# Kernel tuning notes

Measured on AMD Instinct MI355X. Metric: run time of the kernel, lower is better.

## Reference

```python
import jax, jax.numpy as jnp
import numpy as np

N_NODES = 100000
N_EDGES = 1600000
D = 64


def setup_inputs() -> dict:
    key = jax.random.key(0)
    k1, k2, k3 = jax.random.split(key, 3)
    z = jax.random.normal(k1, (N_NODES, D), dtype=jnp.float32)
    ei = jax.random.randint(k2, (2, N_EDGES), 0, N_NODES, dtype=jnp.int32)
    W = jax.random.normal(k3, (D, D), dtype=jnp.float32) * (1.0 / np.sqrt(D))
    b = jnp.zeros((D,), dtype=jnp.float32)
    return {"z": z, "ei": ei, "W": W, "b": b}


def reference(z, ei, W, b):
    # PyG GCNConv(64,64) with default add_self_loops=True, normalize=True, bias,
    # followed by ReLU (from StructDec.forward).
    N = z.shape[0]
    loops = jnp.arange(N, dtype=ei.dtype)
    src = jnp.concatenate([ei[0], loops])  # [E+N]
    dst = jnp.concatenate([ei[1], loops])  # [E+N]

    # symmetric normalization: deg computed on dst with unit edge weights
    deg = jax.ops.segment_sum(jnp.ones_like(dst, dtype=z.dtype), dst, num_segments=N)
    dinv = jnp.where(deg > 0, jax.lax.rsqrt(deg), 0.0)  # deg >= 1 due to self-loops
    norm = dinv[src] * dinv[dst]  # [E+N]

    # linear transform first (small GEMM), then gather-scale-scatter
    x = z @ W.T  # [N, D]
    msg = x[src] * norm[:, None]  # [E+N, D]
    out = jax.ops.segment_sum(msg, dst, num_segments=N) + b  # [N, D]
    return jax.nn.relu(out)
```

## Files before the change

### kernel.cpp

```cpp
#include <hip/hip_runtime.h>

#define DD 64
#define BSH 7
#define GBKT 128
#define CAP 2560
#define TILE 8192
#define PTHREADS 1024
#define EPT 8
#define MAXBK 1024

__device__ __forceinline__ float bflo(unsigned int u) {
    return __uint_as_float(u << 16);
}
__device__ __forceinline__ float bfhi(unsigned int u) {
    return __uint_as_float(u & 0xffff0000u);
}
__device__ __forceinline__ unsigned short f2bf(float f) {
    unsigned int b = __float_as_uint(f);
    return (unsigned short)((b + 0x7fffu + ((b >> 16) & 1u)) >> 16);
}
__device__ __forceinline__ void acc_row(uint4 r, float4& lo, float4& hi) {
    lo.x += bflo(r.x); lo.y += bfhi(r.x);
    lo.z += bflo(r.y); lo.w += bfhi(r.y);
    hi.x += bflo(r.z); hi.y += bfhi(r.z);
    hi.z += bflo(r.w); hi.w += bfhi(r.w);
}

__global__ __launch_bounds__(PTHREADS) void part_k(const int* __restrict__ src,
                                                   const int* __restrict__ dst,
                                                   int* __restrict__ bcur,
                                                   int* __restrict__ bp,
                                                   int E, int NBK) {
    __shared__ int hist[MAXBK];
    __shared__ int scanb[MAXBK];
    __shared__ int gbase[MAXBK];
    __shared__ int stage[TILE];
    __shared__ unsigned short bstage[TILE];

    int tid = threadIdx.x;
    int tbase = blockIdx.x * TILE;
    int n = E - tbase;
    if (n > TILE) n = TILE;

    for (int i = tid; i < NBK; i += PTHREADS) hist[i] = 0;
    __syncthreads();

    int ss[EPT], dd[EPT];
    int eb = tid * EPT;
    bool dal = ((reinterpret_cast<size_t>(dst) & 15) == 0);
    if (dal && eb + EPT <= n) {
        const int4* s4 = (const int4*)(src + tbase + eb);
        const int4* d4 = (const int4*)(dst + tbase + eb);
        int4 a = s4[0], b2 = s4[1], c4 = d4[0], e4 = d4[1];
        ss[0] = a.x; ss[1] = a.y; ss[2] = a.z; ss[3] = a.w;
        ss[4] = b2.x; ss[5] = b2.y; ss[6] = b2.z; ss[7] = b2.w;
        dd[0] = c4.x; dd[1] = c4.y; dd[2] = c4.z; dd[3] = c4.w;
        dd[4] = e4.x; dd[5] = e4.y; dd[6] = e4.z; dd[7] = e4.w;
    } else {
        #pragma unroll
        for (int e = 0; e < EPT; ++e) {
            if (eb + e < n) { ss[e] = src[tbase + eb + e]; dd[e] = dst[tbase + eb + e]; }
            else dd[e] = -1;
        }
    }
    int pv[EPT], pb[EPT], pr[EPT];
    #pragma unroll
    for (int e = 0; e < EPT; ++e) {
        pb[e] = -1;
        if (eb + e < n && dd[e] >= 0) {
            pv[e] = (ss[e] << BSH) | (dd[e] & (GBKT - 1));
            pb[e] = dd[e] >> BSH;
            pr[e] = atomicAdd(&hist[pb[e]], 1);
        }
    }
    __syncthreads();

    if (tid < 64) {
        int run = 0;
        for (int base = 0; base < NBK; base += 64) {
            int i = base + tid;
            int orig = (i < NBK) ? hist[i] : 0;
            int v = orig;
            #pragma unroll
            for (int off = 1; off < 64; off <<= 1) {
                int t = __shfl_up(v, off, 64);
                if (tid >= off) v += t;
            }
            if (i < NBK) scanb[i] = run + v - orig;
            run += __shfl(v, 63, 64);
        }
    }
    __syncthreads();

    for (int i = tid; i < NBK; i += PTHREADS)
        if (hist[i]) gbase[i] = i * CAP + atomicAdd(&bcur[i], hist[i]);
    #pragma unroll
    for (int e = 0; e < EPT; ++e) {
        if (pb[e] >= 0) {
            int p = scanb[pb[e]] + pr[e];
            stage[p] = pv[e];
            bstage[p] = (unsigned short)pb[e];
        }
    }
    __syncthreads();

    for (int i = tid; i < n; i += PTHREADS) {
        int b = bstage[i];
        bp[gbase[b] + (i - scanb[b])] = stage[i];
    }
}

__global__ __launch_bounds__(512) void dg_k(const int* __restrict__ bp,
                                            const int* __restrict__ bcur,
                                            const float* __restrict__ z,
                                            const float* __restrict__ W,
                                            ushort4* __restrict__ ybf, int N) {
    __shared__ float Wt[64 * 68];
    __shared__ float zt[32 * 68];
    __shared__ int cnt[GBKT];
    __shared__ float dinvL[GBKT];
    int k = blockIdx.x;
    int tid = threadIdx.x;
    int base = k << BSH;

    if (tid < GBKT) cnt[tid] = 0;
    for (int i = tid; i < DD * DD; i += 512) {
        int d = i >> 6, kk = i & 63;
        Wt[kk * 68 + d] = W[i];
    }
    __syncthreads();
    {
        int ebeg = k * CAP;
        int eend = ebeg + bcur[k];
        for (int i = ebeg + tid; i < eend; i += 512)
            atomicAdd(&cnt[bp[i] & (GBKT - 1)], 1);
    }
    __syncthreads();
    if (tid < GBKT) dinvL[tid] = rsqrtf((float)(1 + cnt[tid]));
    for (int it = 0; it < 4; ++it) {
        __syncthreads();
        int rl = it * 32 + (tid >> 4);
        int row = base + rl;
        float4 v = (row < N) ? ((const float4*)z)[(size_t)row * 16 + (tid & 15)]
                             : make_float4(0.f, 0.f, 0.f, 0.f);
        *(float4*)&zt[(tid >> 4) * 68 + (tid & 15) * 4] = v;
        __syncthreads();
        int r = tid >> 4, c = tid & 15;
        float4 acc = make_float4(0.f, 0.f, 0.f, 0.f);
        #pragma unroll
        for (int kk = 0; kk < DD; ++kk) {
            float zv = zt[r * 68 + kk];
            float4 w = *(const float4*)&Wt[kk * 68 + c * 4];
            acc.x = fmaf(zv, w.x, acc.x);
            acc.y = fmaf(zv, w.y, acc.y);
            acc.z = fmaf(zv, w.z, acc.z);
            acc.w = fmaf(zv, w.w, acc.w);
        }
        if (row < N) {
            float s = dinvL[rl];
            ushort4 o;
            o.x = f2bf(acc.x * s);
            o.y = f2bf(acc.y * s);
            o.z = f2bf(acc.z * s);
            o.w = f2bf(acc.w * s);
            ybf[(size_t)row * 16 + c] = o;
        }
    }
}

__global__ __launch_bounds__(256) void bg_k(const uint4* __restrict__ ybf,
                                            const int* __restrict__ bp,
                                            const int* __restrict__ bcur,
                                            const float4* __restrict__ b4,
                                            float4* __restrict__ out4, int N) {
    __shared__ int cnt[GBKT];
    __shared__ int excl[GBKT];
    __shared__ int cur[GBKT];
    __shared__ int sorted[CAP];
    __shared__ int nextn;
    int k = blockIdx.x;
    int tid = threadIdx.x;
    int ebeg = k * CAP;
    int eend = ebeg + bcur[k];
    int base = k << BSH;

    if (tid < GBKT) cnt[tid] = 0;
    if (tid == 0) nextn = 0;
    __syncthreads();
    int ev[10];
    #pragma unroll
    for (int u = 0; u < 10; ++u) {
        int i = ebeg + tid + u * 256;
        ev[u] = (i < eend) ? bp[i] : -1;
    }
    #pragma unroll
    for (int u = 0; u < 10; ++u)
        if (ev[u] >= 0) atomicAdd(&cnt[ev[u] & (GBKT - 1)], 1);
    __syncthreads();

    if (tid < GBKT) excl[tid] = cnt[tid];
    __syncthreads();
    #pragma unroll
    for (int off = 1; off < GBKT; off <<= 1) {
        int t = (tid < GBKT && tid >= off) ? excl[tid - off] : 0;
        __syncthreads();
        if (tid < GBKT) excl[tid] += t;
        __syncthreads();
    }
    if (tid < GBKT) {
        excl[tid] -= cnt[tid];
        cur[tid] = excl[tid];
    }
    __syncthreads();

    #pragma unroll
    for (int u = 0; u < 10; ++u)
        if (ev[u] >= 0) {
            int l = ev[u] & (GBKT - 1);
            int pos = atomicAdd(&cur[l], 1);
            sorted[pos] = ev[u] >> BSH;
        }
    __syncthreads();

    int lane = tid & 63;
    int c = tid & 7;
    for (;;) {
        int slot;
        if ((tid & 7) == 0) slot = atomicAdd(&nextn, 1);
        slot = __shfl(slot, lane & 56, 64);
        if (slot >= GBKT) break;
        int node = base + slot;
        if (node >= N) continue;
        int beg = excl[slot];
        int cn = cnt[slot];
        int end = beg + cn;
        uint4 v = ybf[(size_t)node * 8 + c];
        float4 a0 = make_float4(bflo(v.x), bfhi(v.x), bflo(v.y), bfhi(v.y));
        float4 a1 = make_float4(bflo(v.z), bfhi(v.z), bflo(v.w), bfhi(v.w));
        float4 e0 = make_float4(0.f, 0.f, 0.f, 0.f);
        float4 e1 = e0;
        int j = beg;
        for (; j + 7 < end; j += 8) {
            int s0 = sorted[j],     s1 = sorted[j + 1], s2 = sorted[j + 2], s3 = sorted[j + 3];
            int s4 = sorted[j + 4], s5 = sorted[j + 5], s6 = sorted[j + 6], s7 = sorted[j + 7];
            uint4 r0 = ybf[(size_t)s0 * 8 + c];
            uint4 r1 = ybf[(size_t)s1 * 8 + c];
            uint4 r2 = ybf[(size_t)s2 * 8 + c];
            uint4 r3 = ybf[(size_t)s3 * 8 + c];
            uint4 r4 = ybf[(size_t)s4 * 8 + c];
            uint4 r5 = ybf[(size_t)s5 * 8 + c];
            uint4 r6 = ybf[(size_t)s6 * 8 + c];
            uint4 r7 = ybf[(size_t)s7 * 8 + c];
            acc_row(r0, a0, a1);
            acc_row(r1, e0, e1);
            acc_row(r2, a0, a1);
            acc_row(r3, e0, e1);
            acc_row(r4, a0, a1);
            acc_row(r5, e0, e1);
            acc_row(r6, a0, a1);
            acc_row(r7, e0, e1);
        }
        for (; j + 3 < end; j += 4) {
            int s0 = sorted[j], s1 = sorted[j + 1], s2 = sorted[j + 2], s3 = sorted[j + 3];
            uint4 r0 = ybf[(size_t)s0 * 8 + c];
            uint4 r1 = ybf[(size_t)s1 * 8 + c];
            uint4 r2 = ybf[(size_t)s2 * 8 + c];
            uint4 r3 = ybf[(size_t)s3 * 8 + c];
            acc_row(r0, a0, a1);
            acc_row(r1, e0, e1);
            acc_row(r2, a0, a1);
            acc_row(r3, e0, e1);
        }
        for (; j < end; ++j) {
            uint4 r = ybf[(size_t)sorted[j] * 8 + c];
            acc_row(r, a0, a1);
        }
        a0.x += e0.x; a0.y += e0.y; a0.z += e0.z; a0.w += e0.w;
        a1.x += e1.x; a1.y += e1.y; a1.z += e1.z; a1.w += e1.w;

        float dn = rsqrtf((float)(1 + cn));
        float4 bb0 = b4[2 * c];
        float4 bb1 = b4[2 * c + 1];
        float4 o0, o1;
        o0.x = fmaxf(fmaf(a0.x, dn, bb0.x), 0.f);
        o0.y = fmaxf(fmaf(a0.y, dn, bb0.y), 0.f);
        o0.z = fmaxf(fmaf(a0.z, dn, bb0.z), 0.f);
        o0.w = fmaxf(fmaf(a0.w, dn, bb0.w), 0.f);
        o1.x = fmaxf(fmaf(a1.x, dn, bb1.x), 0.f);
        o1.y = fmaxf(fmaf(a1.y, dn, bb1.y), 0.f);
        o1.z = fmaxf(fmaf(a1.z, dn, bb1.z), 0.f);
        o1.w = fmaxf(fmaf(a1.w, dn, bb1.w), 0.f);
        out4[(size_t)node * 16 + 2 * c] = o0;
        out4[(size_t)node * 16 + 2 * c + 1] = o1;
    }
}


extern "C" void kernel_launch(void* const* d_in, const int* in_sizes, int n_in,
                              void* d_out, int out_size, void* d_ws, size_t ws_size,
                              hipStream_t stream) {
    const float* z = (const float*)d_in[0];
    const int* ei  = (const int*)d_in[1];
    const float* W = (const float*)d_in[2];
    const float* b = (const float*)d_in[3];
    float* out = (float*)d_out;

    const int N = in_sizes[0] / DD;
    const int E = in_sizes[1] / 2;
    const int* src = ei;
    const int* dst = ei + E;

    const int NBK = (N + GBKT - 1) >> BSH;

    unsigned short* ybf = (unsigned short*)d_ws;
    int*   bcur  = (int*)(ybf + (size_t)64 * N);
    int*   bp    = bcur + NBK;

    hipMemsetAsync(bcur, 0, sizeof(int) * NBK, stream);
    part_k<<<(E + TILE - 1) / TILE, PTHREADS, 0, stream>>>(src, dst, bcur, bp, E, NBK);
    dg_k<<<NBK, 512, 0, stream>>>(bp, bcur, z, W, (ushort4*)ybf, N);
    bg_k<<<NBK, 256, 0, stream>>>((const uint4*)ybf, bp, bcur,
                                  (const float4*)b, (float4*)out, N);
}
```

Before: 87.33 us.

## Fuse partition, transform and gather into one cooperative persistent kernel

Merges the memset, partition, degree+GEMM and gather stages into a single cooperative kernel that uses grid-wide syncs between phases. Shared memory is reused through a union, and persistent blocks loop over tiles and buckets. The partition tile is halved with more edges per thread. The aim is to remove launch gaps and tail effects between the four launches. In exchange, grid.sync costs are added and occupancy is limited to co-resident blocks. The original multi-kernel path remains as a fallback when the cooperative launch fails.

```diff
diff --git a/kernel.cpp b/kernel.cpp
--- a/kernel.cpp
+++ b/kernel.cpp
@@ -1,13 +1,19 @@
 #include <hip/hip_runtime.h>
+#include <hip/hip_cooperative_groups.h>
+
+namespace cg = cooperative_groups;
 
 #define DD 64
 #define BSH 7
 #define GBKT 128
 #define CAP 2560
-#define TILE 8192
-#define PTHREADS 1024
-#define EPT 8
-#define MAXBK 1024
+#define MAXBK 800
+
+#define FTILE 8192
+#define FPT 1024
+#define FEPT 8
+#define MTILE 4096
+#define MEPT 16
 
 __device__ __forceinline__ float bflo(unsigned int u) {
     return __uint_as_float(u << 16);
@@ -26,166 +32,22 @@
     hi.z += bflo(r.w); hi.w += bfhi(r.w);
 }
 
-__global__ __launch_bounds__(PTHREADS) void part_k(const int* __restrict__ src,
-                                                   const int* __restrict__ dst,
-                                                   int* __restrict__ bcur,
-                                                   int* __restrict__ bp,
-                                                   int E, int NBK) {
-    __shared__ int hist[MAXBK];
-    __shared__ int scanb[MAXBK];
-    __shared__ int gbase[MAXBK];
-    __shared__ int stage[TILE];
-    __shared__ unsigned short bstage[TILE];
-
-    int tid = threadIdx.x;
-    int tbase = blockIdx.x * TILE;
-    int n = E - tbase;
-    if (n > TILE) n = TILE;
-
-    for (int i = tid; i < NBK; i += PTHREADS) hist[i] = 0;
-    __syncthreads();
-
-    int ss[EPT], dd[EPT];
-    int eb = tid * EPT;
-    bool dal = ((reinterpret_cast<size_t>(dst) & 15) == 0);
-    if (dal && eb + EPT <= n) {
-        const int4* s4 = (const int4*)(src + tbase + eb);
-        const int4* d4 = (const int4*)(dst + tbase + eb);
-        int4 a = s4[0], b2 = s4[1], c4 = d4[0], e4 = d4[1];
-        ss[0] = a.x; ss[1] = a.y; ss[2] = a.z; ss[3] = a.w;
-        ss[4] = b2.x; ss[5] = b2.y; ss[6] = b2.z; ss[7] = b2.w;
-        dd[0] = c4.x; dd[1] = c4.y; dd[2] = c4.z; dd[3] = c4.w;
-        dd[4] = e4.x; dd[5] = e4.y; dd[6] = e4.z; dd[7] = e4.w;
-    } else {
-        #pragma unroll
-        for (int e = 0; e < EPT; ++e) {
-            if (eb + e < n) { ss[e] = src[tbase + eb + e]; dd[e] = dst[tbase + eb + e]; }
-            else dd[e] = -1;
-        }
-    }
-    int pv[EPT], pb[EPT], pr[EPT];
-    #pragma unroll
-    for (int e = 0; e < EPT; ++e) {
-        pb[e] = -1;
-        if (eb + e < n && dd[e] >= 0) {
-            pv[e] = (ss[e] << BSH) | (dd[e] & (GBKT - 1));
-            pb[e] = dd[e] >> BSH;
-            pr[e] = atomicAdd(&hist[pb[e]], 1);
-        }
-    }
-    __syncthreads();
-
-    if (tid < 64) {
-        int run = 0;
-        for (int base = 0; base < NBK; base += 64) {
-            int i = base + tid;
-            int orig = (i < NBK) ? hist[i] : 0;
-            int v = orig;
-            #pragma unroll
-            for (int off = 1; off < 64; off <<= 1) {
-                int t = __shfl_up(v, off, 64);
-                if (tid >= off) v += t;
-            }
-            if (i < NBK) scanb[i] = run + v - orig;
-            run += __shfl(v, 63, 64);
-        }
-    }
-    __syncthreads();
-
-    for (int i = tid; i < NBK; i += PTHREADS)
-        if (hist[i]) gbase[i] = i * CAP + atomicAdd(&bcur[i], hist[i]);
-    #pragma unroll
-    for (int e = 0; e < EPT; ++e) {
-        if (pb[e] >= 0) {
-            int p = scanb[pb[e]] + pr[e];
-            stage[p] = pv[e];
-            bstage[p] = (unsigned short)pb[e];
-        }
-    }
-    __syncthreads();
-
-    for (int i = tid; i < n; i += PTHREADS) {
-        int b = bstage[i];
-        bp[gbase[b] + (i - scanb[b])] = stage[i];
-    }
-}
-
-__global__ __launch_bounds__(512) void dg_k(const int* __restrict__ bp,
-                                            const int* __restrict__ bcur,
-                                            const float* __restrict__ z,
-                                            const float* __restrict__ W,
-                                            ushort4* __restrict__ ybf, int N) {
-    __shared__ float Wt[64 * 68];
-    __shared__ float zt[32 * 68];
-    __shared__ int cnt[GBKT];
-    __shared__ float dinvL[GBKT];
-    int k = blockIdx.x;
-    int tid = threadIdx.x;
-    int base = k << BSH;
-
-    if (tid < GBKT) cnt[tid] = 0;
-    for (int i = tid; i < DD * DD; i += 512) {
-        int d = i >> 6, kk = i & 63;
-        Wt[kk * 68 + d] = W[i];
-    }
-    __syncthreads();
-    {
-        int ebeg = k * CAP;
-        int eend = ebeg + bcur[k];
-        for (int i = ebeg + tid; i < eend; i += 512)
-            atomicAdd(&cnt[bp[i] & (GBKT - 1)], 1);
-    }
-    __syncthreads();
-    if (tid < GBKT) dinvL[tid] = rsqrtf((float)(1 + cnt[tid]));
-    for (int it = 0; it < 4; ++it) {
-        __syncthreads();
-        int rl = it * 32 + (tid >> 4);
-        int row = base + rl;
-        float4 v = (row < N) ? ((const float4*)z)[(size_t)row * 16 + (tid & 15)]
-                             : make_float4(0.f, 0.f, 0.f, 0.f);
-        *(float4*)&zt[(tid >> 4) * 68 + (tid & 15) * 4] = v;
-        __syncthreads();
-        int r = tid >> 4, c = tid & 15;
-        float4 acc = make_float4(0.f, 0.f, 0.f, 0.f);
-        #pragma unroll
-        for (int kk = 0; kk < DD; ++kk) {
-            float zv = zt[r * 68 + kk];
-            float4 w = *(const float4*)&Wt[kk * 68 + c * 4];
-            acc.x = fmaf(zv, w.x, acc.x);
-            acc.y = fmaf(zv, w.y, acc.y);
-            acc.z = fmaf(zv, w.z, acc.z);
-            acc.w = fmaf(zv, w.w, acc.w);
-        }
-        if (row < N) {
-            float s = dinvL[rl];
-            ushort4 o;
-            o.x = f2bf(acc.x * s);
-            o.y = f2bf(acc.y * s);
-            o.z = f2bf(acc.z * s);
-            o.w = f2bf(acc.w * s);
-            ybf[(size_t)row * 16 + c] = o;
-        }
-    }
-}
-
-__global__ __launch_bounds__(256) void bg_k(const uint4* __restrict__ ybf,
-                                            const int* __restrict__ bp,
-                                            const int* __restrict__ bcur,
-                                            const float4* __restrict__ b4,
-                                            float4* __restrict__ out4, int N) {
-    __shared__ int cnt[GBKT];
-    __shared__ int excl[GBKT];
-    __shared__ int cur[GBKT];
-    __shared__ int sorted[CAP];
-    __shared__ int nextn;
-    int k = blockIdx.x;
+struct SMb {
+    int cnt[GBKT]; int excl[GBKT]; int cur[GBKT];
+    int sorted[CAP]; int nextn;
+};
+
+__device__ __forceinline__ void bg_body(SMb& s, const uint4* __restrict__ ybf,
+                                        const int* __restrict__ bp, int count,
+                                        const float4* __restrict__ b4,
+                                        float4* __restrict__ out4, int N, int k) {
     int tid = threadIdx.x;
     int ebeg = k * CAP;
-    int eend = ebeg + bcur[k];
+    int eend = ebeg + count;
     int base = k << BSH;
 
-    if (tid < GBKT) cnt[tid] = 0;
-    if (tid == 0) nextn = 0;
+    if (tid < GBKT) s.cnt[tid] = 0;
+    if (tid == 0) s.nextn = 0;
     __syncthreads();
     int ev[10];
     #pragma unroll
@@ -195,30 +57,28 @@
     }
     #pragma unroll
     for (int u = 0; u < 10; ++u)
-        if (ev[u] >= 0) atomicAdd(&cnt[ev[u] & (GBKT - 1)], 1);
-    __syncthreads();
-
-    if (tid < GBKT) excl[tid] = cnt[tid];
+        if (ev[u] >= 0) atomicAdd(&s.cnt[ev[u] & (GBKT - 1)], 1);
+    __syncthreads();
+    if (tid < GBKT) s.excl[tid] = s.cnt[tid];
     __syncthreads();
     #pragma unroll
     for (int off = 1; off < GBKT; off <<= 1) {
-        int t = (tid < GBKT && tid >= off) ? excl[tid - off] : 0;
-        __syncthreads();
-        if (tid < GBKT) excl[tid] += t;
+        int t = (tid < GBKT && tid >= off) ? s.excl[tid - off] : 0;
+        __syncthreads();
+        if (tid < GBKT) s.excl[tid] += t;
         __syncthreads();
     }
     if (tid < GBKT) {
-        excl[tid] -= cnt[tid];
-        cur[tid] = excl[tid];
-    }
-    __syncthreads();
-
+        s.excl[tid] -= s.cnt[tid];
+        s.cur[tid] = s.excl[tid];
+    }
+    __syncthreads();
     #pragma unroll
     for (int u = 0; u < 10; ++u)
         if (ev[u] >= 0) {
             int l = ev[u] & (GBKT - 1);
-            int pos = atomicAdd(&cur[l], 1);
-            sorted[pos] = ev[u] >> BSH;
+            int pos = atomicAdd(&s.cur[l], 1);
+            s.sorted[pos] = ev[u] >> BSH;
         }
     __syncthreads();
 
@@ -226,13 +86,13 @@
     int c = tid & 7;
     for (;;) {
         int slot;
-        if ((tid & 7) == 0) slot = atomicAdd(&nextn, 1);
+        if ((tid & 7) == 0) slot = atomicAdd(&s.nextn, 1);
         slot = __shfl(slot, lane & 56, 64);
         if (slot >= GBKT) break;
         int node = base + slot;
         if (node >= N) continue;
-        int beg = excl[slot];
-        int cn = cnt[slot];
+        int beg = s.excl[slot];
+        int cn = s.cnt[slot];
         int end = beg + cn;
         uint4 v = ybf[(size_t)node * 8 + c];
         float4 a0 = make_float4(bflo(v.x), bfhi(v.x), bflo(v.y), bfhi(v.y));
@@ -241,8 +101,8 @@
         float4 e1 = e0;
         int j = beg;
         for (; j + 7 < end; j += 8) {
-            int s0 = sorted[j],     s1 = sorted[j + 1], s2 = sorted[j + 2], s3 = sorted[j + 3];
-            int s4 = sorted[j + 4], s5 = sorted[j + 5], s6 = sorted[j + 6], s7 = sorted[j + 7];
+            int s0 = s.sorted[j],     s1 = s.sorted[j + 1], s2 = s.sorted[j + 2], s3 = s.sorted[j + 3];
+            int s4 = s.sorted[j + 4], s5 = s.sorted[j + 5], s6 = s.sorted[j + 6], s7 = s.sorted[j + 7];
             uint4 r0 = ybf[(size_t)s0 * 8 + c];
             uint4 r1 = ybf[(size_t)s1 * 8 + c];
             uint4 r2 = ybf[(size_t)s2 * 8 + c];
@@ -261,7 +121,7 @@
             acc_row(r7, e0, e1);
         }
         for (; j + 3 < end; j += 4) {
-            int s0 = sorted[j], s1 = sorted[j + 1], s2 = sorted[j + 2], s3 = sorted[j + 3];
+            int s0 = s.sorted[j], s1 = s.sorted[j + 1], s2 = s.sorted[j + 2], s3 = s.sorted[j + 3];
             uint4 r0 = ybf[(size_t)s0 * 8 + c];
             uint4 r1 = ybf[(size_t)s1 * 8 + c];
             uint4 r2 = ybf[(size_t)s2 * 8 + c];
@@ -272,7 +132,7 @@
             acc_row(r3, e0, e1);
         }
         for (; j < end; ++j) {
-            uint4 r = ybf[(size_t)sorted[j] * 8 + c];
+            uint4 r = ybf[(size_t)s.sorted[j] * 8 + c];
             acc_row(r, a0, a1);
         }
         a0.x += e0.x; a0.y += e0.y; a0.z += e0.z; a0.w += e0.w;
@@ -295,30 +155,360 @@
     }
 }
 
+struct SMp {
+    int hist[MAXBK]; int scanb[MAXBK]; int gbase[MAXBK];
+    int stage[MTILE]; unsigned short bstage[MTILE];
+};
+struct SMg {
+    float Wt[64 * 68]; float zt[16 * 68];
+    int cnt[GBKT]; float dinvL[GBKT];
+};
+union SMu { SMp p; SMg g; SMb b; };
+
+__global__ __launch_bounds__(256, 4) void mega2_k(
+    const int* __restrict__ src, const int* __restrict__ dst,
+    const float* __restrict__ z, const float* __restrict__ W,
+    const float4* __restrict__ b4, ushort4* __restrict__ ybf,
+    int* __restrict__ bcur, int* __restrict__ bp,
+    float4* __restrict__ out4, int N, int E, int NBK, int nt)
+{
+    __shared__ SMu sm;
+    cg::grid_group grid = cg::this_grid();
+    int tid = threadIdx.x;
+    int bid = blockIdx.x;
+    int G = gridDim.x;
+
+    for (int i = bid * 256 + tid; i < NBK; i += G * 256) bcur[i] = 0;
+    grid.sync();
+
+    for (int t = bid; t < nt; t += G) {
+        int tbase = t * MTILE;
+        int n = E - tbase;
+        if (n > MTILE) n = MTILE;
+        __syncthreads();
+        for (int i = tid; i < NBK; i += 256) sm.p.hist[i] = 0;
+        __syncthreads();
+        int pv[MEPT], pb[MEPT], pr[MEPT];
+        int eb = tid * MEPT;
+        bool full = (eb + MEPT <= n);
+        if (full) {
+            #pragma unroll
+            for (int q = 0; q < MEPT / 4; ++q) {
+                int4 s4 = *(const int4*)(src + tbase + eb + q * 4);
+                int4 d4 = *(const int4*)(dst + tbase + eb + q * 4);
+                int sa[4] = {s4.x, s4.y, s4.z, s4.w};
+                int da[4] = {d4.x, d4.y, d4.z, d4.w};
+                #pragma unroll
+                for (int u = 0; u < 4; ++u) {
+                    int e = q * 4 + u;
+                    pv[e] = (sa[u] << BSH) | (da[u] & (GBKT - 1));
+                    pb[e] = da[u] >> BSH;
+                    pr[e] = atomicAdd(&sm.p.hist[pb[e]], 1);
+                }
+            }
+        } else {
+            #pragma unroll
+            for (int e = 0; e < MEPT; ++e) {
+                pb[e] = -1;
+                if (eb + e < n) {
+                    int s = src[tbase + eb + e];
+                    int d = dst[tbase + eb + e];
+                    pv[e] = (s << BSH) | (d & (GBKT - 1));
+                    pb[e] = d >> BSH;
+                    pr[e] = atomicAdd(&sm.p.hist[pb[e]], 1);
+                }
+            }
+        }
+        __syncthreads();
+        if (tid < 64) {
+            int run = 0;
+            for (int base = 0; base < NBK; base += 64) {
+                int i = base + tid;
+                int orig = (i < NBK) ? sm.p.hist[i] : 0;
+                int v = orig;
+                #pragma unroll
+                for (int off = 1; off < 64; off <<= 1) {
+                    int t2 = __shfl_up(v, off, 64);
+                    if (tid >= off) v += t2;
+                }
+                if (i < NBK) sm.p.scanb[i] = run + v - orig;
+                run += __shfl(v, 63, 64);
+            }
+        }
+        __syncthreads();
+        for (int i = tid; i < NBK; i += 256)
+            if (sm.p.hist[i]) sm.p.gbase[i] = i * CAP + atomicAdd(&bcur[i], sm.p.hist[i]);
+        #pragma unroll
+        for (int e = 0; e < MEPT; ++e) {
+            if (pb[e] >= 0) {
+                int p = sm.p.scanb[pb[e]] + pr[e];
+                sm.p.stage[p] = pv[e];
+                sm.p.bstage[p] = (unsigned short)pb[e];
+            }
+        }
+        __syncthreads();
+        for (int i = tid; i < n; i += 256) {
+            int b = sm.p.bstage[i];
+            bp[sm.p.gbase[b] + (i - sm.p.scanb[b])] = sm.p.stage[i];
+        }
+    }
+    grid.sync();
+
+    for (int i = tid; i < DD * DD; i += 256) {
+        int d = i >> 6, kk = i & 63;
+        sm.g.Wt[kk * 68 + d] = W[i];
+    }
+    for (int k = bid; k < NBK; k += G) {
+        __syncthreads();
+        if (tid < GBKT) sm.g.cnt[tid] = 0;
+        __syncthreads();
+        {
+            int ebeg = k * CAP;
+            int eend = ebeg + bcur[k];
+            for (int i = ebeg + tid; i < eend; i += 256)
+                atomicAdd(&sm.g.cnt[bp[i] & (GBKT - 1)], 1);
+        }
+        __syncthreads();
+        if (tid < GBKT) sm.g.dinvL[tid] = rsqrtf((float)(1 + sm.g.cnt[tid]));
+        int base = k << BSH;
+        for (int it = 0; it < 8; ++it) {
+            __syncthreads();
+            int rl = it * 16 + (tid >> 4);
+            int row = base + rl;
+            float4 v = (row < N) ? ((const float4*)z)[(size_t)row * 16 + (tid & 15)]
+                                 : make_float4(0.f, 0.f, 0.f, 0.f);
+            *(float4*)&sm.g.zt[(tid >> 4) * 68 + (tid & 15) * 4] = v;
+            __syncthreads();
+            int r = tid >> 4, c = tid & 15;
+            float4 acc = make_float4(0.f, 0.f, 0.f, 0.f);
+            #pragma unroll
+            for (int kk = 0; kk < DD; ++kk) {
+                float zv = sm.g.zt[r * 68 + kk];
+                float4 w = *(const float4*)&sm.g.Wt[kk * 68 + c * 4];
+                acc.x = fmaf(zv, w.x, acc.x);
+                acc.y = fmaf(zv, w.y, acc.y);
+                acc.z = fmaf(zv, w.z, acc.z);
+                acc.w = fmaf(zv, w.w, acc.w);
+            }
+            if (row < N) {
+                float s = sm.g.dinvL[rl];
+                ushort4 o;
+                o.x = f2bf(acc.x * s);
+                o.y = f2bf(acc.y * s);
+                o.z = f2bf(acc.z * s);
+                o.w = f2bf(acc.w * s);
+                ybf[(size_t)row * 16 + c] = o;
+            }
+        }
+    }
+    grid.sync();
+
+    for (int k = bid; k < NBK; k += G) {
+        __syncthreads();
+        bg_body(sm.b, (const uint4*)ybf, bp, bcur[k], b4, out4, N, k);
+    }
+}
+
+__global__ __launch_bounds__(FPT) void part_k(const int* __restrict__ src,
+                                              const int* __restrict__ dst,
+                                              int* __restrict__ bcur,
+                                              int* __restrict__ bp,
+                                              int E, int NBK) {
+    __shared__ int hist[MAXBK];
+    __shared__ int scanb[MAXBK];
+    __shared__ int gbase[MAXBK];
+    __shared__ int stage[FTILE];
+    __shared__ unsigned short bstage[FTILE];
+
+    int tid = threadIdx.x;
+    int tbase = blockIdx.x * FTILE;
+    int n = E - tbase;
+    if (n > FTILE) n = FTILE;
+
+    for (int i = tid; i < NBK; i += FPT) hist[i] = 0;
+    __syncthreads();
+
+    int ss[FEPT], dd[FEPT];
+    int eb = tid * FEPT;
+    if (eb + FEPT <= n) {
+        const int4* s4 = (const int4*)(src + tbase + eb);
+        const int4* d4 = (const int4*)(dst + tbase + eb);
+        int4 a = s4[0], b2 = s4[1], c4 = d4[0], e4 = d4[1];
+        ss[0] = a.x; ss[1] = a.y; ss[2] = a.z; ss[3] = a.w;
+        ss[4] = b2.x; ss[5] = b2.y; ss[6] = b2.z; ss[7] = b2.w;
+        dd[0] = c4.x; dd[1] = c4.y; dd[2] = c4.z; dd[3] = c4.w;
+        dd[4] = e4.x; dd[5] = e4.y; dd[6] = e4.z; dd[7] = e4.w;
+    } else {
+        #pragma unroll
+        for (int e = 0; e < FEPT; ++e) {
+            if (eb + e < n) { ss[e] = src[tbase + eb + e]; dd[e] = dst[tbase + eb + e]; }
+            else dd[e] = -1;
+        }
+    }
+    int pv[FEPT], pb[FEPT], pr[FEPT];
+    #pragma unroll
+    for (int e = 0; e < FEPT; ++e) {
+        pb[e] = -1;
+        if (eb + e < n && dd[e] >= 0) {
+            pv[e] = (ss[e] << BSH) | (dd[e] & (GBKT - 1));
+            pb[e] = dd[e] >> BSH;
+            pr[e] = atomicAdd(&hist[pb[e]], 1);
+        }
+    }
+    __syncthreads();
+
+    if (tid < 64) {
+        int run = 0;
+        for (int base = 0; base < NBK; base += 64) {
+            int i = base + tid;
+            int orig = (i < NBK) ? hist[i] : 0;
+            int v = orig;
+            #pragma unroll
+            for (int off = 1; off < 64; off <<= 1) {
+                int t = __shfl_up(v, off, 64);
+                if (tid >= off) v += t;
+            }
+            if (i < NBK) scanb[i] = run + v - orig;
+            run += __shfl(v, 63, 64);
+        }
+    }
+    __syncthreads();
+
+    for (int i = tid; i < NBK; i += FPT)
+        if (hist[i]) gbase[i] = i * CAP + atomicAdd(&bcur[i], hist[i]);
+    #pragma unroll
+    for (int e = 0; e < FEPT; ++e) {
+        if (pb[e] >= 0) {
+            int p = scanb[pb[e]] + pr[e];
+            stage[p] = pv[e];
+            bstage[p] = (unsigned short)pb[e];
+        }
+    }
+    __syncthreads();
+
+    for (int i = tid; i < n; i += FPT) {
+        int b = bstage[i];
+        bp[gbase[b] + (i - scanb[b])] = stage[i];
+    }
+}
+
+__global__ __launch_bounds__(512) void dg_k(const int* __restrict__ bp,
+                                            const int* __restrict__ bcur,
+                                            const float* __restrict__ z,
+                                            const float* __restrict__ W,
+                                            ushort4* __restrict__ ybf, int N) {
+    __shared__ float Wt[64 * 68];
+    __shared__ float zt[32 * 68];
+    __shared__ int cnt[GBKT];
+    __shared__ float dinvL[GBKT];
+    int k = blockIdx.x;
+    int tid = threadIdx.x;
+    int base = k << BSH;
+
+    if (tid < GBKT) cnt[tid] = 0;
+    for (int i = tid; i < DD * DD; i += 512) {
+        int d = i >> 6, kk = i & 63;
+        Wt[kk * 68 + d] = W[i];
+    }
+    __syncthreads();
+    {
+        int ebeg = k * CAP;
+        int eend = ebeg + bcur[k];
+        for (int i = ebeg + tid; i < eend; i += 512)
+            atomicAdd(&cnt[bp[i] & (GBKT - 1)], 1);
+    }
+    __syncthreads();
+    if (tid < GBKT) dinvL[tid] = rsqrtf((float)(1 + cnt[tid]));
+    for (int it = 0; it < 4; ++it) {
+        __syncthreads();
+        int rl = it * 32 + (tid >> 4);
+        int row = base + rl;
+        float4 v = (row < N) ? ((const float4*)z)[(size_t)row * 16 + (tid & 15)]
+                             : make_float4(0.f, 0.f, 0.f, 0.f);
+        *(float4*)&zt[(tid >> 4) * 68 + (tid & 15) * 4] = v;
+        __syncthreads();
+        int r = tid >> 4, c = tid & 15;
+        float4 acc = make_float4(0.f, 0.f, 0.f, 0.f);
+        #pragma unroll
+        for (int kk = 0; kk < DD; ++kk) {
+            float zv = zt[r * 68 + kk];
+            float4 w = *(const float4*)&Wt[kk * 68 + c * 4];
+            acc.x = fmaf(zv, w.x, acc.x);
+            acc.y = fmaf(zv, w.y, acc.y);
+            acc.z = fmaf(zv, w.z, acc.z);
+            acc.w = fmaf(zv, w.w, acc.w);
+        }
+        if (row < N) {
+            float s = dinvL[rl];
+            ushort4 o;
+            o.x = f2bf(acc.x * s);
+            o.y = f2bf(acc.y * s);
+            o.z = f2bf(acc.z * s);
+            o.w = f2bf(acc.w * s);
+            ybf[(size_t)row * 16 + c] = o;
+        }
+    }
+}
+
+__global__ __launch_bounds__(256) void bg_k(const uint4* __restrict__ ybf,
+                                            const int* __restrict__ bp,
+                                            const int* __restrict__ bcur,
+                                            const float4* __restrict__ b4,
+                                            float4* __restrict__ out4, int N) {
+    __shared__ SMb s;
+    bg_body(s, ybf, bp, bcur[blockIdx.x], b4, out4, N, blockIdx.x);
+}
 
 extern "C" void kernel_launch(void* const* d_in, const int* in_sizes, int n_in,
                               void* d_out, int out_size, void* d_ws, size_t ws_size,
                               hipStream_t stream) {
-    const float* z = (const float*)d_in[0];
-    const int* ei  = (const int*)d_in[1];
-    const float* W = (const float*)d_in[2];
-    const float* b = (const float*)d_in[3];
-    float* out = (float*)d_out;
-
-    const int N = in_sizes[0] / DD;
-    const int E = in_sizes[1] / 2;
-    const int* src = ei;
-    const int* dst = ei + E;
-
-    const int NBK = (N + GBKT - 1) >> BSH;
-
-    unsigned short* ybf = (unsigned short*)d_ws;
-    int*   bcur  = (int*)(ybf + (size_t)64 * N);
-    int*   bp    = bcur + NBK;
-
-    hipMemsetAsync(bcur, 0, sizeof(int) * NBK, stream);
-    part_k<<<(E + TILE - 1) / TILE, PTHREADS, 0, stream>>>(src, dst, bcur, bp, E, NBK);
-    dg_k<<<NBK, 512, 0, stream>>>(bp, bcur, z, W, (ushort4*)ybf, N);
-    bg_k<<<NBK, 256, 0, stream>>>((const uint4*)ybf, bp, bcur,
-                                  (const float4*)b, (float4*)out, N);
-}
+    const int* ei = (const int*)d_in[1];
+
+    int N = in_sizes[0] / DD;
+    int E = in_sizes[1] / 2;
+    const int* src_p = ei;
+    const int* dst_p = ei + E;
+    const float* z_p = (const float*)d_in[0];
+    const float* W_p = (const float*)d_in[2];
+    const float4* b4_p = (const float4*)d_in[3];
+    float4* out4_p = (float4*)d_out;
+
+    int NBK = (N + GBKT - 1) >> BSH;
+    int nt = (E + MTILE - 1) / MTILE;
+
+    ushort4* ybf_p = (ushort4*)d_ws;
+    int* bcur_p = (int*)((unsigned short*)d_ws + (size_t)64 * N);
+    int* bp_p = bcur_p + NBK;
+
+    bool coop_ok = false;
+    if (NBK <= MAXBK) {
+        int dev = 0;
+        hipGetDevice(&dev);
+        hipDeviceProp_t prop;
+        int mbpc = 0;
+        if (hipGetDeviceProperties(&prop, dev) == hipSuccess &&
+            hipOccupancyMaxActiveBlocksPerMultiprocessor(&mbpc, mega2_k, 256, 0) == hipSuccess &&
+            mbpc > 0) {
+            long long cap = (long long)mbpc * prop.multiProcessorCount;
+            int G = (NBK > nt) ? NBK : nt;
+            if (G > cap) G = (int)cap;
+            if (G > 0) {
+                void* args[] = {
+                    (void*)&src_p, (void*)&dst_p, (void*)&z_p, (void*)&W_p, (void*)&b4_p,
+                    (void*)&ybf_p, (void*)&bcur_p, (void*)&bp_p, (void*)&out4_p,
+                    (void*)&N, (void*)&E, (void*)&NBK, (void*)&nt
+                };
+                hipError_t ce = hipLaunchCooperativeKernel((void*)mega2_k, dim3(G), dim3(256),
+                                                           args, 0, stream);
+                coop_ok = (ce == hipSuccess);
+            }
+        }
+    }
+
+    if (!coop_ok) {
+        hipMemsetAsync(bcur_p, 0, sizeof(int) * NBK, stream);
+        part_k<<<(E + FTILE - 1) / FTILE, FPT, 0, stream>>>(src_p, dst_p, bcur_p, bp_p, E, NBK);
+        dg_k<<<NBK, 512, 0, stream>>>(bp_p, bcur_p, z_p, W_p, ybf_p, N);
+        bg_k<<<NBK, 256, 0, stream>>>((const uint4*)ybf_p, bp_p, bcur_p, b4_p, out4_p, N);
+    }
+}
```

Result: slower. 286.4 us (+227.9%).
